# Optimization experiments

Hardware: AMD Instinct MI355X
Metric: run time of the kernel (lower is better)

## Reference

```python
import jax, jax.numpy as jnp
import numpy as np


def gcn_layer(x, src, dst, deg_inv_sqrt, W, b):
    # PyG GCNConv: h = X W; out[i] = sum_{j->i} norm(j,i) * h[j] + deg_i^{-1} * h[i] + b
    n = x.shape[0]
    h = x @ W                                   # [N, out]
    norm = deg_inv_sqrt[src] * deg_inv_sqrt[dst]  # [E]
    msg = h[src] * norm[:, None]                # [E, out]
    agg = jax.ops.segment_sum(msg, dst, num_segments=n)
    # self-loop contribution (added loops with norm = deg_i^{-1})
    agg = agg + h * (deg_inv_sqrt * deg_inv_sqrt)[:, None]
    return agg + b


def setup_inputs() -> dict:
    key = jax.random.key(0)
    k1, k2, k3, k4, k5, k6 = jax.random.split(key, 6)
    N, E, IN, HID, OUT = 50000, 800000, 128, 128, 64
    x = jax.random.normal(k1, (N, IN), dtype=jnp.float32)
    edge_index = jax.random.randint(k2, (2, E), 0, N, dtype=jnp.int64)
    # glorot-ish init for weights, zeros-ish bias
    W1 = jax.random.normal(k3, (IN, HID), dtype=jnp.float32) * (1.0 / np.sqrt(IN))
    b1 = jax.random.normal(k4, (HID,), dtype=jnp.float32) * 0.01
    W2 = jax.random.normal(k5, (HID, OUT), dtype=jnp.float32) * (1.0 / np.sqrt(HID))
    b2 = jax.random.normal(k6, (OUT,), dtype=jnp.float32) * 0.01
    return {"x": x, "edge_index": edge_index, "W1": W1, "b1": b1, "W2": W2, "b2": b2}


def reference(x, edge_index, W1, b1, W2, b2):
    n = x.shape[0]
    src, dst = edge_index[0], edge_index[1]
    # degree with self-loops (PyG computes degree on the dst/col index)
    deg = jax.ops.segment_sum(jnp.ones_like(dst, dtype=x.dtype), dst, num_segments=n) + 1.0
    deg_inv_sqrt = jax.lax.rsqrt(deg)
    h = gcn_layer(x, src, dst, deg_inv_sqrt, W1, b1)
    h = jax.nn.relu(h)
    # F.dropout with training=False is identity (module evaluated in eval mode)
    out = gcn_layer(h, src, dst, deg_inv_sqrt, W2, b2)
    return out
```

## Files before the change

kernel.cpp:

```cpp
#include <hip/hip_runtime.h>
#include <stdint.h>

typedef __attribute__((ext_vector_type(8))) short short8;
typedef __attribute__((ext_vector_type(4))) float floatx4;

static inline size_t align256(size_t x) { return (x + 255) & ~size_t(255); }

__device__ __forceinline__ unsigned short f2bf(float f) {
    unsigned u = __float_as_uint(f);
    u += 0x7fff + ((u >> 16) & 1);
    return (unsigned short)(u >> 16);
}
__device__ __forceinline__ unsigned pack_bf16(float a, float b) {
    return (unsigned)f2bf(a) | ((unsigned)f2bf(b) << 16);
}
__device__ __forceinline__ float bf_lo(unsigned u) { return __uint_as_float(u << 16); }
__device__ __forceinline__ float bf_hi(unsigned u) { return __uint_as_float(u & 0xffff0000u); }

#define BSHIFT 7
#define NBMAX 1024
#define CH 2048
#define SCAP 3072

__device__ __forceinline__ bool detect_i32(const void* eidx, int E, int t) {
    const long long* e64 = (const long long*)eidx;
    int nchk = E < 256 ? E : 256;
    long long v = e64[t % nchk];
    int bad = (v < 0 || v > 0x7fffffffLL) ? 1 : 0;
    return __syncthreads_or(bad) != 0;
}

__global__ __launch_bounds__(256) void k_hist(const void* __restrict__ eidx, int E,
        int* __restrict__ chist, int NB, int NC,
        const float* __restrict__ W1, const float* __restrict__ W2,
        unsigned short* __restrict__ w1t, unsigned short* __restrict__ w2t,
        int K1, int M1, int K2, int M2) {
    __shared__ int hist[NBMAX];
    const int t = threadIdx.x, B = blockIdx.x;
    if (B < NC) {
        const int e0 = B * CH;
        const int e1 = (e0 + CH < E) ? e0 + CH : E;
        const bool i32 = detect_i32(eidx, E, t);
        const int* e32 = (const int*)eidx;
        const long long* e64 = (const long long*)eidx;
        for (int b0 = 0; b0 < NB; b0 += NBMAX) {
            int bw = (NB - b0 < NBMAX) ? NB - b0 : NBMAX;
            for (int i = t; i < bw; i += 256) hist[i] = 0;
            __syncthreads();
            for (int e = e0 + t; e < e1; e += 256) {
                int d = i32 ? e32[(size_t)E + e] : (int)e64[(size_t)E + e];
                int b = (d >> BSHIFT) - b0;
                if (b >= 0 && b < bw) atomicAdd(&hist[b], 1);
            }
            __syncthreads();
            for (int i = t; i < bw; i += 256) chist[(size_t)(b0 + i) * NC + B] = hist[i];
            __syncthreads();
        }
    } else if (B == NC) {
        for (int j = t; j < K1 * M1; j += 256) {
            int k = j / M1, n = j % M1;
            w1t[(size_t)n * K1 + k] = f2bf(W1[j]);
        }
    } else if (B == NC + 1) {
        for (int j = t; j < K2 * M2; j += 256) {
            int k = j / M2, n = j % M2;
            w2t[(size_t)n * K2 + k] = f2bf(W2[j]);
        }
    }
}

__global__ __launch_bounds__(256) void k_btot(const int* __restrict__ chist,
                                              int* __restrict__ btot, int NB, int NC) {
    int b = blockIdx.x * 4 + (threadIdx.x >> 6);
    if (b >= NB) return;
    int lane = threadIdx.x & 63;
    const int* row = chist + (size_t)b * NC;
    int v = 0;
    for (int i = lane; i < NC; i += 64) v += row[i];
    #pragma unroll
    for (int off = 32; off >= 1; off >>= 1) v += __shfl_xor(v, off, 64);
    if (lane == 0) btot[b] = v;
}

__global__ __launch_bounds__(1024) void k_bscan(const int* __restrict__ btot,
                                                int* __restrict__ bbase,
                                                int* __restrict__ rs_final,
                                                int NB, int N) {
    __shared__ int swt[16];
    const int t = threadIdx.x, lane = t & 63, w = t >> 6;
    int carry = 0;
    for (int base = 0; base < NB; base += 1024) {
        int i = base + t;
        int v = (i < NB) ? btot[i] : 0;
        int incl = v;
        #pragma unroll
        for (int off = 1; off < 64; off <<= 1) {
            int nbr = __shfl_up(incl, off, 64);
            if (lane >= off) incl += nbr;
        }
        if (lane == 63) swt[w] = incl;
        __syncthreads();
        int woff = 0;
        for (int j = 0; j < w; ++j) woff += swt[j];
        if (i < NB) bbase[i] = carry + woff + incl - v;
        int tot = 0;
        for (int j = 0; j < 16; ++j) tot += swt[j];
        carry += tot;
        __syncthreads();
    }
    if (t == 0) { bbase[NB] = carry; rs_final[N] = carry; }
}

__global__ __launch_bounds__(256) void k_hscan2(int* __restrict__ chist,
                                                const int* __restrict__ bbase,
                                                int NB, int NC) {
    int b = blockIdx.x * 4 + (threadIdx.x >> 6);
    if (b >= NB) return;
    int lane = threadIdx.x & 63;
    int* row = chist + (size_t)b * NC;
    int carry = bbase[b];
    for (int base = 0; base < NC; base += 64) {
        int i = base + lane;
        int v = (i < NC) ? row[i] : 0;
        int incl = v;
        #pragma unroll
        for (int off = 1; off < 64; off <<= 1) {
            int nbr = __shfl_up(incl, off, 64);
            if (lane >= off) incl += nbr;
        }
        if (i < NC) row[i] = carry + incl - v;
        carry += __shfl(incl, 63, 64);
    }
}

__global__ __launch_bounds__(256) void k_bfill(const void* __restrict__ eidx, int E,
                                               const int* __restrict__ chist,
                                               uint2* __restrict__ bbuf, int NB, int NC) {
    __shared__ int rank[NBMAX];
    __shared__ int base[NBMAX];
    const int t = threadIdx.x, c = blockIdx.x;
    const int e0 = c * CH;
    const int e1 = (e0 + CH < E) ? e0 + CH : E;
    const bool i32 = detect_i32(eidx, E, t);
    const int* e32 = (const int*)eidx;
    const long long* e64 = (const long long*)eidx;
    for (int b0 = 0; b0 < NB; b0 += NBMAX) {
        int bw = (NB - b0 < NBMAX) ? NB - b0 : NBMAX;
        for (int i = t; i < bw; i += 256) {
            rank[i] = 0;
            base[i] = chist[(size_t)(b0 + i) * NC + c];
        }
        __syncthreads();
        for (int e = e0 + t; e < e1; e += 256) {
            int s, d;
            if (i32) { s = e32[e]; d = e32[(size_t)E + e]; }
            else     { s = (int)e64[e]; d = (int)e64[(size_t)E + e]; }
            int b = (d >> BSHIFT) - b0;
            if (b >= 0 && b < bw) {
                int slot = base[b] + atomicAdd(&rank[b], 1);
                bbuf[slot] = make_uint2((unsigned)s, (unsigned)d);
            }
        }
        __syncthreads();
    }
}

__global__ __launch_bounds__(256) void k_sort(const uint2* __restrict__ bbuf,
                                              const int* __restrict__ bbase,
                                              int* __restrict__ rs_final,
                                              float* __restrict__ dinv,
                                              int* __restrict__ esrc, int N) {
    __shared__ int hist[128];
    __shared__ int off[128];
    __shared__ int srcbuf[SCAP];
    const int b = blockIdx.x, t = threadIdx.x;
    const int node0 = b << BSHIFT;
    const int nloc = (N - node0 < 128) ? N - node0 : 128;
    const int s0 = bbase[b], s1 = bbase[b + 1];
    const int cnt = s1 - s0;
    if (t < 128) hist[t] = 0;
    __syncthreads();
    for (int i = s0 + t; i < s1; i += 256)
        atomicAdd(&hist[bbuf[i].y - (unsigned)node0], 1);
    __syncthreads();
    if (t < 64) {
        int carry = 0;
        #pragma unroll
        for (int base = 0; base < 128; base += 64) {
            int v = hist[base + t];
            int incl = v;
            #pragma unroll
            for (int o = 1; o < 64; o <<= 1) {
                int nbr = __shfl_up(incl, o, 64);
                if (t >= o) incl += nbr;
            }
            off[base + t] = carry + incl - v;
            carry += __shfl(incl, 63, 64);
        }
    }
    __syncthreads();
    if (t < nloc) {
        rs_final[node0 + t] = s0 + off[t];
        dinv[node0 + t] = rsqrtf((float)hist[t] + 1.0f);
    }
    __syncthreads();
    if (t < 128) hist[t] = 0;
    __syncthreads();
    if (cnt <= SCAP) {
        for (int i = s0 + t; i < s1; i += 256) {
            uint2 sd = bbuf[i];
            int lo = sd.y - (unsigned)node0;
            int r = atomicAdd(&hist[lo], 1);
            srcbuf[off[lo] + r] = (int)sd.x;
        }
        __syncthreads();
        for (int i = t; i < cnt; i += 256) esrc[s0 + i] = srcbuf[i];
    } else {
        for (int i = s0 + t; i < s1; i += 256) {
            uint2 sd = bbuf[i];
            int lo = sd.y - (unsigned)node0;
            int r = atomicAdd(&hist[lo], 1);
            esrc[s0 + off[lo] + r] = (int)sd.x;
        }
    }
}

template<int BN, bool AF32>
__global__ __launch_bounds__(256, 3) void k_gemm(
        const void* __restrict__ Av, const unsigned short* __restrict__ Bt,
        const float* __restrict__ dinv, unsigned short* __restrict__ C,
        int N, int M) {
    constexpr int LD = 136;
    __shared__ unsigned short As[64 * LD];
    __shared__ unsigned short Bs[BN * LD];
    const int tid = threadIdx.x;
    const int wave = tid >> 6, lane = tid & 63;
    const int q = lane >> 4, tm = lane & 15;
    const int row0 = blockIdx.x * 64;

    {
        const uint4* Bg = (const uint4*)Bt;
        #pragma unroll
        for (int it = 0; it < BN / 16; ++it) {
            int i = tid + it * 256;
            int r = i >> 4, o = i & 15;
            *(uint4*)&Bs[r * LD + o * 8] = Bg[(size_t)r * 16 + o];
        }
    }
    if (AF32) {
        const float4* Ag = (const float4*)Av;
        #pragma unroll
        for (int it = 0; it < 8; ++it) {
            int i = tid + it * 256;
            int r = i >> 5, o = i & 31;
            int row = row0 + r;
            float4 v = make_float4(0.f, 0.f, 0.f, 0.f);
            if (row < N) v = Ag[(size_t)row * 32 + o];
            uint2 pk;
            pk.x = pack_bf16(v.x, v.y);
            pk.y = pack_bf16(v.z, v.w);
            *(uint2*)&As[r * LD + o * 4] = pk;
        }
    } else {
        const uint4* Ag = (const uint4*)Av;
        #pragma unroll
        for (int it = 0; it < 4; ++it) {
            int i = tid + it * 256;
            int r = i >> 4, o = i & 15;
            int row = row0 + r;
            uint4 v = make_uint4(0, 0, 0, 0);
            if (row < N) v = Ag[(size_t)row * 16 + o];
            *(uint4*)&As[r * LD + o * 8] = v;
        }
    }
    __syncthreads();

    constexpr int NG = BN / 16;
    floatx4 acc[NG];
    #pragma unroll
    for (int g = 0; g < NG; ++g) acc[g] = (floatx4){0.f, 0.f, 0.f, 0.f};

    const int arow = wave * 16 + tm;
    #pragma unroll
    for (int kc = 0; kc < 4; ++kc) {
        short8 af = *(const short8*)&As[arow * LD + kc * 32 + q * 8];
        #pragma unroll
        for (int g = 0; g < NG; ++g) {
            short8 bf = *(const short8*)&Bs[(g * 16 + tm) * LD + kc * 32 + q * 8];
            acc[g] = __builtin_amdgcn_mfma_f32_16x16x32_bf16(af, bf, acc[g], 0, 0, 0);
        }
    }

    float dv[4];
    #pragma unroll
    for (int r = 0; r < 4; ++r) {
        int row = row0 + wave * 16 + q * 4 + r;
        dv[r] = (row < N) ? dinv[row] : 0.f;
    }
    #pragma unroll
    for (int g = 0; g < NG; ++g) {
        #pragma unroll
        for (int r = 0; r < 4; ++r) {
            int row = row0 + wave * 16 + q * 4 + r;
            if (row < N) C[(size_t)row * M + g * 16 + tm] = f2bf(dv[r] * acc[g][r]);
        }
    }
}

__global__ __launch_bounds__(256) void k_agg128(const unsigned* __restrict__ Hb,
        const float* __restrict__ dinv, const int* __restrict__ rs,
        const int* __restrict__ esrc, const float* __restrict__ bias,
        unsigned* __restrict__ out, int N) {
    int wid = (blockIdx.x * 256 + threadIdx.x) >> 6;
    if (wid >= N) return;
    int l = threadIdx.x & 63;
    float di = dinv[wid];
    unsigned a = Hb[(size_t)wid * 64 + l];
    float accx = bf_lo(a), accy = bf_hi(a);
    int k = rs[wid], kend = rs[wid + 1];
    for (; k + 8 <= kend; k += 8) {
        int s[8];
        #pragma unroll
        for (int j = 0; j < 8; ++j) s[j] = esrc[k + j];
        unsigned g[8];
        #pragma unroll
        for (int j = 0; j < 8; ++j) g[j] = Hb[(size_t)s[j] * 64 + l];
        #pragma unroll
        for (int j = 0; j < 8; ++j) { accx += bf_lo(g[j]); accy += bf_hi(g[j]); }
    }
    if (k + 4 <= kend) {
        int s[4];
        #pragma unroll
        for (int j = 0; j < 4; ++j) s[j] = esrc[k + j];
        unsigned g[4];
        #pragma unroll
        for (int j = 0; j < 4; ++j) g[j] = Hb[(size_t)s[j] * 64 + l];
        #pragma unroll
        for (int j = 0; j < 4; ++j) { accx += bf_lo(g[j]); accy += bf_hi(g[j]); }
        k += 4;
    }
    for (; k < kend; ++k) {
        unsigned g = Hb[(size_t)esrc[k] * 64 + l];
        accx += bf_lo(g); accy += bf_hi(g);
    }
    float2 b = ((const float2*)bias)[l];
    float ox = fmaxf(fmaf(di, accx, b.x), 0.f);
    float oy = fmaxf(fmaf(di, accy, b.y), 0.f);
    out[(size_t)wid * 64 + l] = pack_bf16(ox, oy);
}

__global__ __launch_bounds__(256) void k_agg64(const unsigned short* __restrict__ Hb,
        const float* __restrict__ dinv, const int* __restrict__ rs,
        const int* __restrict__ esrc, const float* __restrict__ bias,
        float* __restrict__ out, int N) {
    int wid = (blockIdx.x * 256 + threadIdx.x) >> 6;
    if (wid >= N) return;
    int l = threadIdx.x & 63;
    float di = dinv[wid];
    float acc = __uint_as_float((unsigned)Hb[(size_t)wid * 64 + l] << 16);
    int k = rs[wid], kend = rs[wid + 1];
    for (; k + 8 <= kend; k += 8) {
        int s[8];
        #pragma unroll
        for (int j = 0; j < 8; ++j) s[j] = esrc[k + j];
        unsigned short g[8];
        #pragma unroll
        for (int j = 0; j < 8; ++j) g[j] = Hb[(size_t)s[j] * 64 + l];
        #pragma unroll
        for (int j = 0; j < 8; ++j) acc += __uint_as_float((unsigned)g[j] << 16);
    }
    if (k + 4 <= kend) {
        int s[4];
        #pragma unroll
        for (int j = 0; j < 4; ++j) s[j] = esrc[k + j];
        unsigned short g[4];
        #pragma unroll
        for (int j = 0; j < 4; ++j) g[j] = Hb[(size_t)s[j] * 64 + l];
        #pragma unroll
        for (int j = 0; j < 4; ++j) acc += __uint_as_float((unsigned)g[j] << 16);
        k += 4;
    }
    for (; k < kend; ++k)
        acc += __uint_as_float((unsigned)Hb[(size_t)esrc[k] * 64 + l] << 16);
    out[(size_t)wid * 64 + l] = fmaf(di, acc, bias[l]);
}

extern "C" void kernel_launch(void* const* d_in, const int* in_sizes, int n_in,
                              void* d_out, int out_size, void* d_ws, size_t ws_size,
                              hipStream_t stream) {
    const float* x  = (const float*)d_in[0];
    const void*  ei = d_in[1];
    const float* W1 = (const float*)d_in[2];
    const float* b1 = (const float*)d_in[3];
    const float* W2 = (const float*)d_in[4];
    const float* b2 = (const float*)d_in[5];

    int HID = in_sizes[3];
    int IN  = in_sizes[2] / HID;
    int OUT = in_sizes[4] / HID;
    int N   = in_sizes[0] / IN;
    int E   = in_sizes[1] / 2;
    int NB  = (N + 127) >> BSHIFT;
    int NC  = (E + CH - 1) / CH;

    char* p = (char*)d_ws;
    int* chist     = (int*)p;   p += align256((size_t)NB * NC * 4);
    int* btot      = (int*)p;   p += align256((size_t)NB * 4);
    int* bbase     = (int*)p;   p += align256((size_t)(NB + 1) * 4);
    int* rs_final  = (int*)p;   p += align256((size_t)(N + 1) * 4);
    int* esrc      = (int*)p;   p += align256((size_t)E * 4);
    float* dinv    = (float*)p; p += align256((size_t)N * 4);
    unsigned short* w1t = (unsigned short*)p; p += align256((size_t)HID * IN * 2);
    unsigned short* w2t = (unsigned short*)p; p += align256((size_t)OUT * HID * 2);
    size_t hb_bytes = (size_t)N * HID * 2, bbuf_bytes = (size_t)E * 8;
    uint2* bbuf    = (uint2*)p;
    unsigned short* hb = (unsigned short*)p;
    p += align256(hb_bytes > bbuf_bytes ? hb_bytes : bbuf_bytes);
    unsigned short* h1b = (unsigned short*)p; p += align256((size_t)N * HID * 2);
    unsigned short* h2b = (unsigned short*)p; p += align256((size_t)N * OUT * 2);

    k_hist<<<NC + 2, 256, 0, stream>>>(ei, E, chist, NB, NC,
                                       W1, W2, w1t, w2t, IN, HID, HID, OUT);
    k_btot<<<(NB + 3) / 4, 256, 0, stream>>>(chist, btot, NB, NC);
    k_bscan<<<1, 1024, 0, stream>>>(btot, bbase, rs_final, NB, N);
    k_hscan2<<<(NB + 3) / 4, 256, 0, stream>>>(chist, bbase, NB, NC);
    k_bfill<<<NC, 256, 0, stream>>>(ei, E, chist, bbuf, NB, NC);
    k_sort<<<NB, 256, 0, stream>>>(bbuf, bbase, rs_final, dinv, esrc, N);

    k_gemm<128, true><<<(N + 63) / 64, 256, 0, stream>>>(x, w1t, dinv, hb, N, HID);
    k_agg128<<<(N + 3) / 4, 256, 0, stream>>>((unsigned*)hb, dinv, rs_final, esrc, b1,
                                              (unsigned*)h1b, N);

    k_gemm<64, false><<<(N + 63) / 64, 256, 0, stream>>>(h1b, w2t, dinv, h2b, N, OUT);
    k_agg64<<<(N + 3) / 4, 256, 0, stream>>>(h2b, dinv, rs_final, esrc, b2, (float*)d_out, N);
}
```

Measured before the change: 208.1 us.

## Fuse bucket totals into scan, pack edge pairs to 32 bits, unroll gathers

Three changes. The bucket-total kernel is merged into the single-block scan, which drops one launch but serialises about 391x25 reads onto one workgroup. Bucketed edges are packed into 32 bits, the local destination in the top 7 bits and the source in the low 25, which halves bbuf traffic in the fill and sort kernels. The aggregation loops are unrolled to 16 gathers in flight to raise memory-level parallelism. The fused scan now assumes NB is at most 1024, and the packing assumes N is below 2^25.

```diff
diff --git a/kernel.cpp b/kernel.cpp
--- a/kernel.cpp
+++ b/kernel.cpp
@@ -69,46 +69,39 @@
     }
 }
 
-__global__ __launch_bounds__(256) void k_btot(const int* __restrict__ chist,
-                                              int* __restrict__ btot, int NB, int NC) {
-    int b = blockIdx.x * 4 + (threadIdx.x >> 6);
-    if (b >= NB) return;
-    int lane = threadIdx.x & 63;
-    const int* row = chist + (size_t)b * NC;
-    int v = 0;
-    for (int i = lane; i < NC; i += 64) v += row[i];
-    #pragma unroll
-    for (int off = 32; off >= 1; off >>= 1) v += __shfl_xor(v, off, 64);
-    if (lane == 0) btot[b] = v;
-}
-
-__global__ __launch_bounds__(1024) void k_bscan(const int* __restrict__ btot,
+__global__ __launch_bounds__(1024) void k_bscan(const int* __restrict__ chist,
                                                 int* __restrict__ bbase,
                                                 int* __restrict__ rs_final,
-                                                int NB, int N) {
+                                                int NB, int NC, int N) {
+    __shared__ int tot[1024];
     __shared__ int swt[16];
     const int t = threadIdx.x, lane = t & 63, w = t >> 6;
-    int carry = 0;
-    for (int base = 0; base < NB; base += 1024) {
-        int i = base + t;
-        int v = (i < NB) ? btot[i] : 0;
-        int incl = v;
-        #pragma unroll
-        for (int off = 1; off < 64; off <<= 1) {
-            int nbr = __shfl_up(incl, off, 64);
-            if (lane >= off) incl += nbr;
-        }
-        if (lane == 63) swt[w] = incl;
-        __syncthreads();
-        int woff = 0;
-        for (int j = 0; j < w; ++j) woff += swt[j];
-        if (i < NB) bbase[i] = carry + woff + incl - v;
-        int tot = 0;
-        for (int j = 0; j < 16; ++j) tot += swt[j];
-        carry += tot;
-        __syncthreads();
-    }
-    if (t == 0) { bbase[NB] = carry; rs_final[N] = carry; }
+    for (int b = w; b < NB; b += 16) {
+        const int* row = chist + (size_t)b * NC;
+        int v = 0;
+        for (int i = lane; i < NC; i += 64) v += row[i];
+        #pragma unroll
+        for (int off = 32; off >= 1; off >>= 1) v += __shfl_xor(v, off, 64);
+        if (lane == 0) tot[b] = v;
+    }
+    __syncthreads();
+    int v = (t < NB) ? tot[t] : 0;
+    int incl = v;
+    #pragma unroll
+    for (int off = 1; off < 64; off <<= 1) {
+        int nbr = __shfl_up(incl, off, 64);
+        if (lane >= off) incl += nbr;
+    }
+    if (lane == 63) swt[w] = incl;
+    __syncthreads();
+    int woff = 0;
+    for (int j = 0; j < w; ++j) woff += swt[j];
+    if (t < NB) bbase[t] = woff + incl - v;
+    if (t == 1023) {
+        int total = woff + incl;
+        bbase[NB] = total;
+        rs_final[N] = total;
+    }
 }
 
 __global__ __launch_bounds__(256) void k_hscan2(int* __restrict__ chist,
@@ -135,7 +128,7 @@
 
 __global__ __launch_bounds__(256) void k_bfill(const void* __restrict__ eidx, int E,
                                                const int* __restrict__ chist,
-                                               uint2* __restrict__ bbuf, int NB, int NC) {
+                                               unsigned* __restrict__ bbuf, int NB, int NC) {
     __shared__ int rank[NBMAX];
     __shared__ int base[NBMAX];
     const int t = threadIdx.x, c = blockIdx.x;
@@ -158,14 +151,14 @@
             int b = (d >> BSHIFT) - b0;
             if (b >= 0 && b < bw) {
                 int slot = base[b] + atomicAdd(&rank[b], 1);
-                bbuf[slot] = make_uint2((unsigned)s, (unsigned)d);
+                bbuf[slot] = ((unsigned)(d & 127) << 25) | (unsigned)s;
             }
         }
         __syncthreads();
     }
 }
 
-__global__ __launch_bounds__(256) void k_sort(const uint2* __restrict__ bbuf,
+__global__ __launch_bounds__(256) void k_sort(const unsigned* __restrict__ bbuf,
                                               const int* __restrict__ bbase,
                                               int* __restrict__ rs_final,
                                               float* __restrict__ dinv,
@@ -181,7 +174,7 @@
     if (t < 128) hist[t] = 0;
     __syncthreads();
     for (int i = s0 + t; i < s1; i += 256)
-        atomicAdd(&hist[bbuf[i].y - (unsigned)node0], 1);
+        atomicAdd(&hist[bbuf[i] >> 25], 1);
     __syncthreads();
     if (t < 64) {
         int carry = 0;
@@ -208,19 +201,19 @@
     __syncthreads();
     if (cnt <= SCAP) {
         for (int i = s0 + t; i < s1; i += 256) {
-            uint2 sd = bbuf[i];
-            int lo = sd.y - (unsigned)node0;
+            unsigned sd = bbuf[i];
+            int lo = sd >> 25;
             int r = atomicAdd(&hist[lo], 1);
-            srcbuf[off[lo] + r] = (int)sd.x;
+            srcbuf[off[lo] + r] = (int)(sd & 0x1ffffffu);
         }
         __syncthreads();
         for (int i = t; i < cnt; i += 256) esrc[s0 + i] = srcbuf[i];
     } else {
         for (int i = s0 + t; i < s1; i += 256) {
-            uint2 sd = bbuf[i];
-            int lo = sd.y - (unsigned)node0;
+            unsigned sd = bbuf[i];
+            int lo = sd >> 25;
             int r = atomicAdd(&hist[lo], 1);
-            esrc[s0 + off[lo] + r] = (int)sd.x;
+            esrc[s0 + off[lo] + r] = (int)(sd & 0x1ffffffu);
         }
     }
 }
@@ -318,7 +311,17 @@
     unsigned a = Hb[(size_t)wid * 64 + l];
     float accx = bf_lo(a), accy = bf_hi(a);
     int k = rs[wid], kend = rs[wid + 1];
-    for (; k + 8 <= kend; k += 8) {
+    for (; k + 16 <= kend; k += 16) {
+        int s[16];
+        #pragma unroll
+        for (int j = 0; j < 16; ++j) s[j] = esrc[k + j];
+        unsigned g[16];
+        #pragma unroll
+        for (int j = 0; j < 16; ++j) g[j] = Hb[(size_t)s[j] * 64 + l];
+        #pragma unroll
+        for (int j = 0; j < 16; ++j) { accx += bf_lo(g[j]); accy += bf_hi(g[j]); }
+    }
+    if (k + 8 <= kend) {
         int s[8];
         #pragma unroll
         for (int j = 0; j < 8; ++j) s[j] = esrc[k + j];
@@ -327,6 +330,7 @@
         for (int j = 0; j < 8; ++j) g[j] = Hb[(size_t)s[j] * 64 + l];
         #pragma unroll
         for (int j = 0; j < 8; ++j) { accx += bf_lo(g[j]); accy += bf_hi(g[j]); }
+        k += 8;
     }
     if (k + 4 <= kend) {
         int s[4];
@@ -359,7 +363,17 @@
     float di = dinv[wid];
     float acc = __uint_as_float((unsigned)Hb[(size_t)wid * 64 + l] << 16);
     int k = rs[wid], kend = rs[wid + 1];
-    for (; k + 8 <= kend; k += 8) {
+    for (; k + 16 <= kend; k += 16) {
+        int s[16];
+        #pragma unroll
+        for (int j = 0; j < 16; ++j) s[j] = esrc[k + j];
+        unsigned short g[16];
+        #pragma unroll
+        for (int j = 0; j < 16; ++j) g[j] = Hb[(size_t)s[j] * 64 + l];
+        #pragma unroll
+        for (int j = 0; j < 16; ++j) acc += __uint_as_float((unsigned)g[j] << 16);
+    }
+    if (k + 8 <= kend) {
         int s[8];
         #pragma unroll
         for (int j = 0; j < 8; ++j) s[j] = esrc[k + j];
@@ -368,6 +382,7 @@
         for (int j = 0; j < 8; ++j) g[j] = Hb[(size_t)s[j] * 64 + l];
         #pragma unroll
         for (int j = 0; j < 8; ++j) acc += __uint_as_float((unsigned)g[j] << 16);
+        k += 8;
     }
     if (k + 4 <= kend) {
         int s[4];
@@ -405,15 +420,14 @@
 
     char* p = (char*)d_ws;
     int* chist     = (int*)p;   p += align256((size_t)NB * NC * 4);
-    int* btot      = (int*)p;   p += align256((size_t)NB * 4);
     int* bbase     = (int*)p;   p += align256((size_t)(NB + 1) * 4);
     int* rs_final  = (int*)p;   p += align256((size_t)(N + 1) * 4);
     int* esrc      = (int*)p;   p += align256((size_t)E * 4);
     float* dinv    = (float*)p; p += align256((size_t)N * 4);
     unsigned short* w1t = (unsigned short*)p; p += align256((size_t)HID * IN * 2);
     unsigned short* w2t = (unsigned short*)p; p += align256((size_t)OUT * HID * 2);
-    size_t hb_bytes = (size_t)N * HID * 2, bbuf_bytes = (size_t)E * 8;
-    uint2* bbuf    = (uint2*)p;
+    size_t hb_bytes = (size_t)N * HID * 2, bbuf_bytes = (size_t)E * 4;
+    unsigned* bbuf = (unsigned*)p;
     unsigned short* hb = (unsigned short*)p;
     p += align256(hb_bytes > bbuf_bytes ? hb_bytes : bbuf_bytes);
     unsigned short* h1b = (unsigned short*)p; p += align256((size_t)N * HID * 2);
@@ -421,8 +435,7 @@
 
     k_hist<<<NC + 2, 256, 0, stream>>>(ei, E, chist, NB, NC,
                                        W1, W2, w1t, w2t, IN, HID, HID, OUT);
-    k_btot<<<(NB + 3) / 4, 256, 0, stream>>>(chist, btot, NB, NC);
-    k_bscan<<<1, 1024, 0, stream>>>(btot, bbase, rs_final, NB, N);
+    k_bscan<<<1, 1024, 0, stream>>>(chist, bbase, rs_final, NB, NC, N);
     k_hscan2<<<(NB + 3) / 4, 256, 0, stream>>>(chist, bbase, NB, NC);
     k_bfill<<<NC, 256, 0, stream>>>(ei, E, chist, bbuf, NB, NC);
     k_sort<<<NB, 256, 0, stream>>>(bbuf, bbase, rs_final, dinv, esrc, N);
```

Result: slower. 236.9 us (+13.9%).
